# Performance work log

Measured on AMD Instinct MI355X. Metric: run time of the kernel, lower is better.

The kernel has to match this reference:

```python
import jax, jax.numpy as jnp
import numpy as np

B, S, F, OWN, H, E = 16384, 37, 17, 9, 256, 128
NOUT = 7 + 16


def setup_inputs() -> dict:
    key = jax.random.key(0)
    ks = jax.random.split(key, 22)
    obs = jax.random.normal(ks[0], (B, S + 1, F), dtype=jnp.float32)
    pad = jax.random.bernoulli(ks[1], 0.3, (B, S))
    obs = obs.at[:, 1:, :].multiply(jnp.where(pad, 0.0, 1.0)[:, :, None])

    def init(k, shape):
        return jax.random.normal(k, shape, dtype=jnp.float32) * 0.05

    params = dict(
        sW1=init(ks[2], (F, H)), sb1=jnp.zeros((H,), jnp.float32),
        sW2=init(ks[3], (H, H)), sb2=jnp.zeros((H,), jnp.float32),
        sW3=init(ks[4], (H, E)), sb3=jnp.zeros((E,), jnp.float32),
        aW1=init(ks[5], (E + OWN, H)), ab1=jnp.zeros((H,), jnp.float32),
        aW2=init(ks[6], (H, H)), ab2=jnp.zeros((H,), jnp.float32),
        aW3=init(ks[7], (H, NOUT)), ab3=jnp.zeros((NOUT,), jnp.float32),
        vW1=init(ks[8], (E + OWN, H)), vb1=jnp.zeros((H,), jnp.float32),
        vW2=init(ks[9], (H, H)), vb2=jnp.zeros((H,), jnp.float32),
        vW3=init(ks[10], (H, 1)), vb3=jnp.zeros((1,), jnp.float32),
    )
    return {"obs": obs, **params}


def reference(obs, sW1, sb1, sW2, sb2, sW3, sb3,
              aW1, ab1, aW2, ab2, aW3, ab3,
              vW1, vb1, vW2, vb2, vW3, vb3):
    s_own = obs[:, 0, :OWN]                      # [B, 9]
    seqs = obs[:, 1:, :]                         # [B, 37, 17]
    # non-padded mask: rows whose abs-sum is nonzero
    mask = (jnp.sum(jnp.abs(seqs), axis=-1) != 0).astype(obs.dtype)  # [B, 37]

    # shared MLP applied to every row; masked positions zeroed before the
    # pooling sum (equivalent to gather->MLP->scatter into zeros->sum)
    h = jax.nn.relu(seqs @ sW1 + sb1)
    h = jax.nn.relu(h @ sW2 + sb2)
    h = jax.nn.relu(h @ sW3 + sb3)               # [B, 37, E]
    h = h * mask[..., None]
    summed = jnp.sum(h, axis=1)                  # [B, E]

    cat = jnp.concatenate([summed, s_own], axis=1)  # [B, E+9]

    a = jax.nn.relu(cat @ aW1 + ab1)
    a = jax.nn.relu(a @ aW2 + ab2)
    action_logits = a @ aW3 + ab3                # [B, 23]

    v = jax.nn.relu(cat @ vW1 + vb1)
    v = jax.nn.relu(v @ vW2 + vb2)
    value = (v @ vW3 + vb3).reshape(-1)          # [B]

    return action_logits, value
```

## Files before the change

kernel.cpp:

```cpp
#include <hip/hip_runtime.h>
#include <hip/hip_bf16.h>

#define B_    16384
#define S_    37
#define F_    17
#define OWN_  9
#define NOUT_ 23
#define OBS_ROW 646

typedef __bf16 bf16x8 __attribute__((ext_vector_type(8)));
typedef float  f32x4  __attribute__((ext_vector_type(4)));

#define MFMA(a,b,c) __builtin_amdgcn_mfma_f32_16x16x32_bf16(a, b, c, 0, 0, 0)

#define W1F_OFF   0
#define W2F_OFF   8192
#define W3F_OFF   73728
#define AW1F_OFF  106496
#define AW2F_OFF  147456
#define AW3F_OFF  212992
#define VW1F_OFF  221184
#define VW2F_OFF  262144
#define VW3F_OFF  327680
#define PREP_TOTAL 331776

__global__ void prep_kernel(const float* __restrict__ sW1, const float* __restrict__ sW2,
                            const float* __restrict__ sW3, const float* __restrict__ aW1,
                            const float* __restrict__ aW2, const float* __restrict__ aW3,
                            const float* __restrict__ vW1, const float* __restrict__ vW2,
                            const float* __restrict__ vW3, __bf16* __restrict__ ws)
{
    int j = blockIdx.x * 256 + threadIdx.x;
    const float* src; __bf16* dst; int Np, Ks, Ns;
    if (j < 8192)                  { dst = ws + W1F_OFF;  src = sW1; Np = 256; Ks = 17;  Ns = 256; }
    else if ((j -= 8192)  < 65536) { dst = ws + W2F_OFF;  src = sW2; Np = 256; Ks = 256; Ns = 256; }
    else if ((j -= 65536) < 32768) { dst = ws + W3F_OFF;  src = sW3; Np = 128; Ks = 256; Ns = 128; }
    else if ((j -= 32768) < 40960) { dst = ws + AW1F_OFF; src = aW1; Np = 256; Ks = 137; Ns = 256; }
    else if ((j -= 40960) < 65536) { dst = ws + AW2F_OFF; src = aW2; Np = 256; Ks = 256; Ns = 256; }
    else if ((j -= 65536) < 8192)  { dst = ws + AW3F_OFF; src = aW3; Np = 32;  Ks = 256; Ns = 23;  }
    else if ((j -= 8192)  < 40960) { dst = ws + VW1F_OFF; src = vW1; Np = 256; Ks = 137; Ns = 256; }
    else if ((j -= 40960) < 65536) { dst = ws + VW2F_OFF; src = vW2; Np = 256; Ks = 256; Ns = 256; }
    else { j -= 65536;               dst = ws + VW3F_OFF; src = vW3; Np = 16;  Ks = 256; Ns = 1;   }
    const int c = j / (Np * 8), rem = j - c * Np * 8, n = rem >> 3, e = rem & 7, k = c * 8 + e;
    const float v = (k < Ks && n < Ns) ? src[k * Ns + n] : 0.f;
    dst[j] = (__bf16)v;
}

__global__ __launch_bounds__(512, 2) void fused_kernel(
    const float* __restrict__ obs,
    const float* __restrict__ sb1, const float* __restrict__ sb2, const float* __restrict__ sb3,
    const float* __restrict__ ab1, const float* __restrict__ ab2, const float* __restrict__ ab3,
    const float* __restrict__ vb1, const float* __restrict__ vb2, const float* __restrict__ vb3,
    const __bf16* __restrict__ ws, float* __restrict__ out)
{
    __shared__ __align__(16) char pool[74240];
    __bf16* act1 = (__bf16*)pool;
    __bf16* act2 = (__bf16*)(pool + 32768);
    __bf16* xs0  = (__bf16*)(pool + 65536);
    __bf16* xs1  = (__bf16*)(pool + 69632);
    float*  sm0  = (float*)(pool + 73728);
    float*  sm1  = (float*)(pool + 73984);
    __bf16* catf = (__bf16*)(pool + 65536);

    const __bf16* W1f  = ws + W1F_OFF;
    const __bf16* W2f  = ws + W2F_OFF;
    const __bf16* W3f  = ws + W3F_OFF;
    const __bf16* AW1f = ws + AW1F_OFF;
    const __bf16* AW2f = ws + AW2F_OFF;
    const __bf16* AW3f = ws + AW3F_OFF;
    const __bf16* VW1f = ws + VW1F_OFF;
    const __bf16* VW2f = ws + VW2F_OFF;
    const __bf16* VW3f = ws + VW3F_OFF;

    const int tid  = threadIdx.x;
    const int wave = tid >> 6;
    const int lane = tid & 63;
    const int q    = lane >> 4;
    const int l16  = lane & 15;
    const int b0   = blockIdx.x * 16;
    const f32x4 z4 = {0.f, 0.f, 0.f, 0.f};

    for (int i = tid; i < 4096; i += 512) xs0[i] = (__bf16)0.f;

    bf16x8 w1f[2], w2f[8][2], w3f[8];
    float b1v[2], b2v[2];
    #pragma unroll
    for (int nt = 0; nt < 2; ++nt) {
        const int n = wave * 32 + nt * 16 + l16;
        w1f[nt] = *(const bf16x8*)(W1f + ((size_t)q * 256 + n) * 8);
        b1v[nt] = sb1[n];
        b2v[nt] = sb2[n];
        #pragma unroll
        for (int k = 0; k < 8; ++k)
            w2f[k][nt] = *(const bf16x8*)(W2f + ((size_t)(k * 4 + q) * 256 + n) * 8);
    }
    #pragma unroll
    for (int k = 0; k < 8; ++k)
        w3f[k] = *(const bf16x8*)(W3f + ((size_t)(k * 4 + q) * 128 + wave * 16 + l16) * 8);
    const float b3v = sb3[wave * 16 + l16];

    __syncthreads();

    if (wave == 7) {
        const float* p = obs + (size_t)(b0 + (lane & 15)) * OBS_ROW + ((lane >> 4) + 1) * F_;
        float sm = 0.f;
        #pragma unroll
        for (int c = 0; c < F_; ++c) {
            const float v = p[c];
            sm += fabsf(v);
            xs0[((c >> 3) * 64 + lane) * 8 + (c & 7)] = (__bf16)v;
        }
        sm0[lane] = sm;
    }

    f32x4 vsum = z4;

    for (int it = 0; it < 10; ++it) {
        __bf16* xc  = (it & 1) ? xs1 : xs0;
        __bf16* xn  = (it & 1) ? xs0 : xs1;
        float*  smc = (it & 1) ? sm1 : sm0;
        float*  smn = (it & 1) ? sm0 : sm1;

        __syncthreads();

        if (it < 9 && wave == 7) {
            const int s = 4 * (it + 1) + (lane >> 4);
            if (s < S_) {
                const float* p = obs + (size_t)(b0 + (lane & 15)) * OBS_ROW + (s + 1) * F_;
                float sm = 0.f;
                #pragma unroll
                for (int c = 0; c < F_; ++c) {
                    const float v = p[c];
                    sm += fabsf(v);
                    xn[((c >> 3) * 64 + lane) * 8 + (c & 7)] = (__bf16)v;
                }
                smn[lane] = sm;
            } else {
                smn[lane] = 0.f;
            }
        }

        {
            #pragma unroll
            for (int m = 0; m < 4; ++m) {
                const bf16x8 af = *(const bf16x8*)(xc + (q * 64 + m * 16 + l16) * 8);
                #pragma unroll
                for (int nt = 0; nt < 2; ++nt) {
                    const f32x4 h = MFMA(af, w1f[nt], z4);
                    const int n = wave * 32 + nt * 16 + l16, c = n >> 3, e = n & 7;
                    #pragma unroll
                    for (int r = 0; r < 4; ++r) {
                        float v = h[r] + b1v[nt]; v = v > 0.f ? v : 0.f;
                        act1[(c * 64 + m * 16 + q * 4 + r) * 8 + e] = (__bf16)v;
                    }
                }
            }
        }
        __syncthreads();

        {
            f32x4 h2[2][4];
            #pragma unroll
            for (int nt = 0; nt < 2; ++nt)
                #pragma unroll
                for (int m = 0; m < 4; ++m) h2[nt][m] = z4;
            #pragma unroll
            for (int k = 0; k < 8; ++k) {
                const int k8 = k * 4 + q;
                #pragma unroll
                for (int m = 0; m < 4; ++m) {
                    const bf16x8 a = *(const bf16x8*)(act1 + (k8 * 64 + m * 16 + l16) * 8);
                    h2[0][m] = MFMA(a, w2f[k][0], h2[0][m]);
                    h2[1][m] = MFMA(a, w2f[k][1], h2[1][m]);
                }
            }
            #pragma unroll
            for (int nt = 0; nt < 2; ++nt) {
                const int n = wave * 32 + nt * 16 + l16, c = n >> 3, e = n & 7;
                #pragma unroll
                for (int m = 0; m < 4; ++m)
                    #pragma unroll
                    for (int r = 0; r < 4; ++r) {
                        float v = h2[nt][m][r] + b2v[nt]; v = v > 0.f ? v : 0.f;
                        act2[(c * 64 + m * 16 + q * 4 + r) * 8 + e] = (__bf16)v;
                    }
            }
        }
        __syncthreads();

        {
            f32x4 h3[4];
            #pragma unroll
            for (int m = 0; m < 4; ++m) h3[m] = z4;
            #pragma unroll
            for (int k = 0; k < 8; ++k) {
                const int k8 = k * 4 + q;
                #pragma unroll
                for (int m = 0; m < 4; ++m) {
                    const bf16x8 a = *(const bf16x8*)(act2 + (k8 * 64 + m * 16 + l16) * 8);
                    h3[m] = MFMA(a, w3f[k], h3[m]);
                }
            }
            #pragma unroll
            for (int m = 0; m < 4; ++m)
                #pragma unroll
                for (int r = 0; r < 4; ++r) {
                    const float mv = smc[m * 16 + q * 4 + r];
                    float v = h3[m][r] + b3v;
                    v = v > 0.f ? v : 0.f;
                    vsum[r] += (mv != 0.f) ? v : 0.f;
                }
    }
    }

    __syncthreads();

    if (tid < 16) {
        const float* p = obs + (size_t)(b0 + tid) * OBS_ROW;
        #pragma unroll
        for (int c = 0; c < 8; ++c) catf[(16 * 16 + tid) * 8 + c] = (__bf16)p[c];
        catf[(17 * 16 + tid) * 8 + 0] = (__bf16)p[8];
        #pragma unroll
        for (int c = 1; c < 8; ++c) catf[(17 * 16 + tid) * 8 + c] = (__bf16)0.f;
    } else if (tid < 32) {
        const int rr = tid - 16;
        #pragma unroll
        for (int c = 0; c < 8; ++c) {
            catf[(18 * 16 + rr) * 8 + c] = (__bf16)0.f;
            catf[(19 * 16 + rr) * 8 + c] = (__bf16)0.f;
        }
    }
    {
        const int col = wave * 16 + l16, c = col >> 3, e = col & 7;
        #pragma unroll
        for (int r = 0; r < 4; ++r)
            catf[(c * 16 + q * 4 + r) * 8 + e] = (__bf16)vsum[r];
    }
    __syncthreads();

    {
        f32x4 ha[2], hv[2];
        #pragma unroll
        for (int nt = 0; nt < 2; ++nt) { ha[nt] = z4; hv[nt] = z4; }
        #pragma unroll
        for (int k = 0; k < 5; ++k) {
            const int k8 = k * 4 + q;
            const bf16x8 ca = *(const bf16x8*)(catf + (k8 * 16 + l16) * 8);
            #pragma unroll
            for (int nt = 0; nt < 2; ++nt) {
                const int n = wave * 32 + nt * 16 + l16;
                const bf16x8 ba = *(const bf16x8*)(AW1f + ((size_t)k8 * 256 + n) * 8);
                const bf16x8 bv = *(const bf16x8*)(VW1f + ((size_t)k8 * 256 + n) * 8);
                ha[nt] = MFMA(ca, ba, ha[nt]);
                hv[nt] = MFMA(ca, bv, hv[nt]);
            }
        }
        #pragma unroll
        for (int nt = 0; nt < 2; ++nt) {
            const int n = wave * 32 + nt * 16 + l16, c = n >> 3, e = n & 7;
            const float ba_ = ab1[n], bv_ = vb1[n];
            #pragma unroll
            for (int r = 0; r < 4; ++r) {
                float va = ha[nt][r] + ba_; va = va > 0.f ? va : 0.f;
                float vv = hv[nt][r] + bv_; vv = vv > 0.f ? vv : 0.f;
                act1[(c * 64 + q * 4 + r) * 8 + e]      = (__bf16)va;
                act1[(c * 64 + 16 + q * 4 + r) * 8 + e] = (__bf16)vv;
            }
        }
    }
    __syncthreads();

    {
        f32x4 ha[2], hv[2];
        #pragma unroll
        for (int nt = 0; nt < 2; ++nt) { ha[nt] = z4; hv[nt] = z4; }
        #pragma unroll
        for (int k = 0; k < 8; ++k) {
            const int k8 = k * 4 + q;
            const bf16x8 a0 = *(const bf16x8*)(act1 + (k8 * 64 + l16) * 8);
            const bf16x8 a1 = *(const bf16x8*)(act1 + (k8 * 64 + 16 + l16) * 8);
            #pragma unroll
            for (int nt = 0; nt < 2; ++nt) {
                const int n = wave * 32 + nt * 16 + l16;
                const bf16x8 ba = *(const bf16x8*)(AW2f + ((size_t)k8 * 256 + n) * 8);
                const bf16x8 bv = *(const bf16x8*)(VW2f + ((size_t)k8 * 256 + n) * 8);
                ha[nt] = MFMA(a0, ba, ha[nt]);
                hv[nt] = MFMA(a1, bv, hv[nt]);
            }
        }
        #pragma unroll
        for (int nt = 0; nt < 2; ++nt) {
            const int n = wave * 32 + nt * 16 + l16, c = n >> 3, e = n & 7;
            const float ba_ = ab2[n], bv_ = vb2[n];
            #pragma unroll
            for (int r = 0; r < 4; ++r) {
                float va = ha[nt][r] + ba_; va = va > 0.f ? va : 0.f;
                float vv = hv[nt][r] + bv_; vv = vv > 0.f ? vv : 0.f;
                act2[(c * 64 + q * 4 + r) * 8 + e]      = (__bf16)va;
                act2[(c * 64 + 16 + q * 4 + r) * 8 + e] = (__bf16)vv;
            }
        }
    }
    __syncthreads();

    if (wave < 2) {
        f32x4 acc = z4;
        #pragma unroll
        for (int k = 0; k < 8; ++k) {
            const int k8 = k * 4 + q;
            const bf16x8 a0 = *(const bf16x8*)(act2 + (k8 * 64 + l16) * 8);
            const bf16x8 bf = *(const bf16x8*)(AW3f + ((size_t)k8 * 32 + wave * 16 + l16) * 8);
            acc = MFMA(a0, bf, acc);
        }
        const int col = wave * 16 + l16;
        if (col < NOUT_) {
            const float bb = ab3[col];
            #pragma unroll
            for (int r = 0; r < 4; ++r)
                out[(size_t)(b0 + q * 4 + r) * NOUT_ + col] = acc[r] + bb;
        }
    } else if (wave == 2) {
        f32x4 acc = z4;
        #pragma unroll
        for (int k = 0; k < 8; ++k) {
            const int k8 = k * 4 + q;
            const bf16x8 a1 = *(const bf16x8*)(act2 + (k8 * 64 + 16 + l16) * 8);
            const bf16x8 bf = *(const bf16x8*)(VW3f + ((size_t)k8 * 16 + l16) * 8);
            acc = MFMA(a1, bf, acc);
        }
        if (l16 == 0) {
            const float bb = vb3[0];
            #pragma unroll
            for (int r = 0; r < 4; ++r)
                out[(size_t)B_ * NOUT_ + b0 + q * 4 + r] = acc[r] + bb;
        }
    }
}

extern "C" void kernel_launch(void* const* d_in, const int* in_sizes, int n_in,
                              void* d_out, int out_size, void* d_ws, size_t ws_size,
                              hipStream_t stream)
{
    const float* obs = (const float*)d_in[0];
    const float* sW1 = (const float*)d_in[1];
    const float* sb1 = (const float*)d_in[2];
    const float* sW2 = (const float*)d_in[3];
    const float* sb2 = (const float*)d_in[4];
    const float* sW3 = (const float*)d_in[5];
    const float* sb3 = (const float*)d_in[6];
    const float* aW1 = (const float*)d_in[7];
    const float* ab1 = (const float*)d_in[8];
    const float* aW2 = (const float*)d_in[9];
    const float* ab2 = (const float*)d_in[10];
    const float* aW3 = (const float*)d_in[11];
    const float* ab3 = (const float*)d_in[12];
    const float* vW1 = (const float*)d_in[13];
    const float* vb1 = (const float*)d_in[14];
    const float* vW2 = (const float*)d_in[15];
    const float* vb2 = (const float*)d_in[16];
    const float* vW3 = (const float*)d_in[17];
    const float* vb3 = (const float*)d_in[18];

    __bf16* ws = (__bf16*)d_ws;
    float* out = (float*)d_out;

    hipLaunchKernelGGL(prep_kernel, dim3(PREP_TOTAL / 256), dim3(256), 0, stream,
                       sW1, sW2, sW3, aW1, aW2, aW3, vW1, vW2, vW3, ws);
    hipLaunchKernelGGL(fused_kernel, dim3(B_ / 16), dim3(512), 0, stream,
                       obs, sb1, sb2, sb3, ab1, ab2, ab3, vb1, vb2, vb3,
                       (const __bf16*)ws, out);
}
```

Baseline: 283.6 us.

## Preload all obs rows into LDS, transpose MFMA operands, split layer-3 over row halves

All ten groups of neighbor rows for the block are now loaded into shared memory up front, replacing the double-buffered producer wave. The MFMA operand order is swapped so each lane holds four consecutive output features, which allows packed 4-wide bf16 LDS stores and vectorised bias loads. Layer 3 is split so waves cover 32 columns by two row halves, with the partial sums combined through shared memory. This cuts scalar LDS stores and removes the idle producer wave, but raises LDS use to about 107 KB, which may reduce blocks per CU below the launch bound of 2, and the obs load is no longer overlapped with compute.

New measurement: 265.8 us. -6.3%, faster.

```diff
diff --git a/kernel.cpp b/kernel.cpp
--- a/kernel.cpp
+++ b/kernel.cpp
@@ -9,6 +9,7 @@
 #define OBS_ROW 646
 
 typedef __bf16 bf16x8 __attribute__((ext_vector_type(8)));
+typedef __bf16 bf16x4 __attribute__((ext_vector_type(4)));
 typedef float  f32x4  __attribute__((ext_vector_type(4)));
 
 #define MFMA(a,b,c) __builtin_amdgcn_mfma_f32_16x16x32_bf16(a, b, c, 0, 0, 0)
@@ -53,14 +54,13 @@
     const float* __restrict__ vb1, const float* __restrict__ vb2, const float* __restrict__ vb3,
     const __bf16* __restrict__ ws, float* __restrict__ out)
 {
-    __shared__ __align__(16) char pool[74240];
-    __bf16* act1 = (__bf16*)pool;
-    __bf16* act2 = (__bf16*)(pool + 32768);
-    __bf16* xs0  = (__bf16*)(pool + 65536);
-    __bf16* xs1  = (__bf16*)(pool + 69632);
-    float*  sm0  = (float*)(pool + 73728);
-    float*  sm1  = (float*)(pool + 73984);
-    __bf16* catf = (__bf16*)(pool + 65536);
+    __shared__ __align__(16) char pool[109056];
+    __bf16* act1    = (__bf16*)pool;
+    __bf16* act2    = (__bf16*)(pool + 32768);
+    __bf16* xs_full = (__bf16*)(pool + 65536);
+    float*  sm_full = (float*)(pool + 106496);
+    __bf16* catf    = (__bf16*)(pool + 65536);
+    float*  partial = (float*)pool;
 
     const __bf16* W1f  = ws + W1F_OFF;
     const __bf16* W2f  = ws + W2F_OFF;
@@ -77,144 +77,139 @@
     const int lane = tid & 63;
     const int q    = lane >> 4;
     const int l16  = lane & 15;
+    const int qh   = q >> 1;
+    const int e4   = (q & 1) * 4;
     const int b0   = blockIdx.x * 16;
+    const int nc   = wave & 3;
+    const int mr   = wave >> 2;
     const f32x4 z4 = {0.f, 0.f, 0.f, 0.f};
 
-    for (int i = tid; i < 4096; i += 512) xs0[i] = (__bf16)0.f;
-
-    bf16x8 w1f[2], w2f[8][2], w3f[8];
-    float b1v[2], b2v[2];
+    #pragma unroll
+    for (int i = 0; i < 5; ++i)
+        ((f32x4*)xs_full)[tid + i * 512] = z4;
+
+    bf16x8 w1f[2], w2f[8][2], w3f[2][8];
+    f32x4 b1q[2], b2q[2], b3q[2];
     #pragma unroll
     for (int nt = 0; nt < 2; ++nt) {
         const int n = wave * 32 + nt * 16 + l16;
         w1f[nt] = *(const bf16x8*)(W1f + ((size_t)q * 256 + n) * 8);
-        b1v[nt] = sb1[n];
-        b2v[nt] = sb2[n];
-        #pragma unroll
-        for (int k = 0; k < 8; ++k)
+        b1q[nt] = *(const f32x4*)(sb1 + wave * 32 + nt * 16 + q * 4);
+        b2q[nt] = *(const f32x4*)(sb2 + wave * 32 + nt * 16 + q * 4);
+        b3q[nt] = *(const f32x4*)(sb3 + nc * 32 + nt * 16 + q * 4);
+        #pragma unroll
+        for (int k = 0; k < 8; ++k) {
             w2f[k][nt] = *(const bf16x8*)(W2f + ((size_t)(k * 4 + q) * 256 + n) * 8);
-    }
-    #pragma unroll
-    for (int k = 0; k < 8; ++k)
-        w3f[k] = *(const bf16x8*)(W3f + ((size_t)(k * 4 + q) * 128 + wave * 16 + l16) * 8);
-    const float b3v = sb3[wave * 16 + l16];
-
-    __syncthreads();
-
-    if (wave == 7) {
-        const float* p = obs + (size_t)(b0 + (lane & 15)) * OBS_ROW + ((lane >> 4) + 1) * F_;
+            w3f[nt][k] = *(const bf16x8*)(W3f + ((size_t)(k * 4 + q) * 128 + nc * 32 + nt * 16 + l16) * 8);
+        }
+    }
+
+    __syncthreads();
+
+    for (int rr = tid; rr < 640; rr += 512) {
+        const int g = rr >> 6, tr = rr & 63, b = tr & 15, sl = tr >> 4;
+        const int s = g * 4 + sl;
         float sm = 0.f;
-        #pragma unroll
-        for (int c = 0; c < F_; ++c) {
-            const float v = p[c];
-            sm += fabsf(v);
-            xs0[((c >> 3) * 64 + lane) * 8 + (c & 7)] = (__bf16)v;
-        }
-        sm0[lane] = sm;
-    }
-
-    f32x4 vsum = z4;
+        if (s < S_) {
+            const float* p = obs + (size_t)(b0 + b) * OBS_ROW + (s + 1) * F_;
+            #pragma unroll
+            for (int c = 0; c < F_; ++c) {
+                const float v = p[c];
+                sm += fabsf(v);
+                xs_full[g * 2048 + ((c >> 3) * 64 + tr) * 8 + (c & 7)] = (__bf16)v;
+            }
+        }
+        sm_full[rr] = sm;
+    }
+
+    __syncthreads();
+
+    f32x4 vsum[2] = {z4, z4};
 
     for (int it = 0; it < 10; ++it) {
-        __bf16* xc  = (it & 1) ? xs1 : xs0;
-        __bf16* xn  = (it & 1) ? xs0 : xs1;
-        float*  smc = (it & 1) ? sm1 : sm0;
-        float*  smn = (it & 1) ? sm0 : sm1;
-
+        const __bf16* xg  = xs_full + it * 2048;
+        const float*  smg = sm_full + it * 64;
+
+        #pragma unroll
+        for (int m = 0; m < 4; ++m) {
+            const bf16x8 xm = *(const bf16x8*)(xg + (q * 64 + m * 16 + l16) * 8);
+            #pragma unroll
+            for (int nt = 0; nt < 2; ++nt) {
+                const f32x4 h = MFMA(w1f[nt], xm, z4);
+                float v0 = h[0] + b1q[nt][0]; v0 = v0 > 0.f ? v0 : 0.f;
+                float v1 = h[1] + b1q[nt][1]; v1 = v1 > 0.f ? v1 : 0.f;
+                float v2 = h[2] + b1q[nt][2]; v2 = v2 > 0.f ? v2 : 0.f;
+                float v3 = h[3] + b1q[nt][3]; v3 = v3 > 0.f ? v3 : 0.f;
+                const bf16x4 pk = {(__bf16)v0, (__bf16)v1, (__bf16)v2, (__bf16)v3};
+                *(bf16x4*)(act1 + ((wave * 4 + nt * 2 + qh) * 64 + m * 16 + l16) * 8 + e4) = pk;
+            }
+        }
         __syncthreads();
 
-        if (it < 9 && wave == 7) {
-            const int s = 4 * (it + 1) + (lane >> 4);
-            if (s < S_) {
-                const float* p = obs + (size_t)(b0 + (lane & 15)) * OBS_ROW + (s + 1) * F_;
-                float sm = 0.f;
-                #pragma unroll
-                for (int c = 0; c < F_; ++c) {
-                    const float v = p[c];
-                    sm += fabsf(v);
-                    xn[((c >> 3) * 64 + lane) * 8 + (c & 7)] = (__bf16)v;
+        {
+            f32x4 h2[2][4];
+            #pragma unroll
+            for (int nt = 0; nt < 2; ++nt)
+                #pragma unroll
+                for (int m = 0; m < 4; ++m) h2[nt][m] = z4;
+            #pragma unroll
+            for (int k = 0; k < 8; ++k) {
+                const int k8 = k * 4 + q;
+                #pragma unroll
+                for (int m = 0; m < 4; ++m) {
+                    const bf16x8 a = *(const bf16x8*)(act1 + (k8 * 64 + m * 16 + l16) * 8);
+                    h2[0][m] = MFMA(w2f[k][0], a, h2[0][m]);
+                    h2[1][m] = MFMA(w2f[k][1], a, h2[1][m]);
                 }
-                smn[lane] = sm;
-            } else {
-                smn[lane] = 0.f;
-            }
-        }
+            }
+            #pragma unroll
+            for (int nt = 0; nt < 2; ++nt)
+                #pragma unroll
+                for (int m = 0; m < 4; ++m) {
+                    float v0 = h2[nt][m][0] + b2q[nt][0]; v0 = v0 > 0.f ? v0 : 0.f;
+                    float v1 = h2[nt][m][1] + b2q[nt][1]; v1 = v1 > 0.f ? v1 : 0.f;
+                    float v2 = h2[nt][m][2] + b2q[nt][2]; v2 = v2 > 0.f ? v2 : 0.f;
+                    float v3 = h2[nt][m][3] + b2q[nt][3]; v3 = v3 > 0.f ? v3 : 0.f;
+                    const bf16x4 pk = {(__bf16)v0, (__bf16)v1, (__bf16)v2, (__bf16)v3};
+                    *(bf16x4*)(act2 + ((wave * 4 + nt * 2 + qh) * 64 + m * 16 + l16) * 8 + e4) = pk;
+                }
+        }
+        __syncthreads();
 
         {
-            #pragma unroll
-            for (int m = 0; m < 4; ++m) {
-                const bf16x8 af = *(const bf16x8*)(xc + (q * 64 + m * 16 + l16) * 8);
-                #pragma unroll
-                for (int nt = 0; nt < 2; ++nt) {
-                    const f32x4 h = MFMA(af, w1f[nt], z4);
-                    const int n = wave * 32 + nt * 16 + l16, c = n >> 3, e = n & 7;
+            f32x4 h3[2][2] = {{z4, z4}, {z4, z4}};
+            #pragma unroll
+            for (int k = 0; k < 8; ++k) {
+                const int k8 = k * 4 + q;
+                #pragma unroll
+                for (int mi = 0; mi < 2; ++mi) {
+                    const bf16x8 a = *(const bf16x8*)(act2 + (k8 * 64 + (mr * 2 + mi) * 16 + l16) * 8);
+                    h3[0][mi] = MFMA(w3f[0][k], a, h3[0][mi]);
+                    h3[1][mi] = MFMA(w3f[1][k], a, h3[1][mi]);
+                }
+            }
+            #pragma unroll
+            for (int mi = 0; mi < 2; ++mi) {
+                const float mk = (smg[(mr * 2 + mi) * 16 + l16] != 0.f) ? 1.f : 0.f;
+                #pragma unroll
+                for (int nt = 0; nt < 2; ++nt)
                     #pragma unroll
                     for (int r = 0; r < 4; ++r) {
-                        float v = h[r] + b1v[nt]; v = v > 0.f ? v : 0.f;
-                        act1[(c * 64 + m * 16 + q * 4 + r) * 8 + e] = (__bf16)v;
+                        float v = h3[nt][mi][r] + b3q[nt][r];
+                        v = v > 0.f ? v : 0.f;
+                        vsum[nt][r] += mk * v;
                     }
-                }
-            }
-        }
-        __syncthreads();
-
-        {
-            f32x4 h2[2][4];
-            #pragma unroll
-            for (int nt = 0; nt < 2; ++nt)
-                #pragma unroll
-                for (int m = 0; m < 4; ++m) h2[nt][m] = z4;
-            #pragma unroll
-            for (int k = 0; k < 8; ++k) {
-                const int k8 = k * 4 + q;
-                #pragma unroll
-                for (int m = 0; m < 4; ++m) {
-                    const bf16x8 a = *(const bf16x8*)(act1 + (k8 * 64 + m * 16 + l16) * 8);
-                    h2[0][m] = MFMA(a, w2f[k][0], h2[0][m]);
-                    h2[1][m] = MFMA(a, w2f[k][1], h2[1][m]);
-                }
-            }
-            #pragma unroll
-            for (int nt = 0; nt < 2; ++nt) {
-                const int n = wave * 32 + nt * 16 + l16, c = n >> 3, e = n & 7;
-                #pragma unroll
-                for (int m = 0; m < 4; ++m)
-                    #pragma unroll
-                    for (int r = 0; r < 4; ++r) {
-                        float v = h2[nt][m][r] + b2v[nt]; v = v > 0.f ? v : 0.f;
-                        act2[(c * 64 + m * 16 + q * 4 + r) * 8 + e] = (__bf16)v;
-                    }
-            }
-        }
-        __syncthreads();
-
-        {
-            f32x4 h3[4];
-            #pragma unroll
-            for (int m = 0; m < 4; ++m) h3[m] = z4;
-            #pragma unroll
-            for (int k = 0; k < 8; ++k) {
-                const int k8 = k * 4 + q;
-                #pragma unroll
-                for (int m = 0; m < 4; ++m) {
-                    const bf16x8 a = *(const bf16x8*)(act2 + (k8 * 64 + m * 16 + l16) * 8);
-                    h3[m] = MFMA(a, w3f[k], h3[m]);
-                }
-            }
-            #pragma unroll
-            for (int m = 0; m < 4; ++m)
-                #pragma unroll
-                for (int r = 0; r < 4; ++r) {
-                    const float mv = smc[m * 16 + q * 4 + r];
-                    float v = h3[m][r] + b3v;
-                    v = v > 0.f ? v : 0.f;
-                    vsum[r] += (mv != 0.f) ? v : 0.f;
-                }
-    }
-    }
-
-    __syncthreads();
-
+            }
+        }
+    }
+
+    if (mr == 0) {
+        #pragma unroll
+        for (int nt = 0; nt < 2; ++nt)
+            #pragma unroll
+            for (int r = 0; r < 4; ++r)
+                partial[(nc * 32 + nt * 16 + q * 4 + r) * 16 + l16] = vsum[nt][r];
+    }
     if (tid < 16) {
         const float* p = obs + (size_t)(b0 + tid) * OBS_ROW;
         #pragma unroll
@@ -230,18 +225,23 @@
             catf[(19 * 16 + rr) * 8 + c] = (__bf16)0.f;
         }
     }
+    __syncthreads();
+
+    if (mr == 1) {
+        #pragma unroll
+        for (int nt = 0; nt < 2; ++nt) {
+            f32x4 t = vsum[nt];
+            #pragma unroll
+            for (int r = 0; r < 4; ++r)
+                t[r] += partial[(nc * 32 + nt * 16 + q * 4 + r) * 16 + l16];
+            const bf16x4 pk = {(__bf16)t[0], (__bf16)t[1], (__bf16)t[2], (__bf16)t[3]};
+            *(bf16x4*)(catf + ((nc * 4 + nt * 2 + qh) * 16 + l16) * 8 + e4) = pk;
+        }
+    }
+    __syncthreads();
+
     {
-        const int col = wave * 16 + l16, c = col >> 3, e = col & 7;
-        #pragma unroll
-        for (int r = 0; r < 4; ++r)
-            catf[(c * 16 + q * 4 + r) * 8 + e] = (__bf16)vsum[r];
-    }
-    __syncthreads();
-
-    {
-        f32x4 ha[2], hv[2];
-        #pragma unroll
-        for (int nt = 0; nt < 2; ++nt) { ha[nt] = z4; hv[nt] = z4; }
+        f32x4 ha[2] = {z4, z4}, hv[2] = {z4, z4};
         #pragma unroll
         for (int k = 0; k < 5; ++k) {
             const int k8 = k * 4 + q;
@@ -251,29 +251,33 @@
                 const int n = wave * 32 + nt * 16 + l16;
                 const bf16x8 ba = *(const bf16x8*)(AW1f + ((size_t)k8 * 256 + n) * 8);
                 const bf16x8 bv = *(const bf16x8*)(VW1f + ((size_t)k8 * 256 + n) * 8);
-                ha[nt] = MFMA(ca, ba, ha[nt]);
-                hv[nt] = MFMA(ca, bv, hv[nt]);
+                ha[nt] = MFMA(ba, ca, ha[nt]);
+                hv[nt] = MFMA(bv, ca, hv[nt]);
             }
         }
         #pragma unroll
         for (int nt = 0; nt < 2; ++nt) {
-            const int n = wave * 32 + nt * 16 + l16, c = n >> 3, e = n & 7;
-            const float ba_ = ab1[n], bv_ = vb1[n];
-            #pragma unroll
-            for (int r = 0; r < 4; ++r) {
-                float va = ha[nt][r] + ba_; va = va > 0.f ? va : 0.f;
-                float vv = hv[nt][r] + bv_; vv = vv > 0.f ? vv : 0.f;
-                act1[(c * 64 + q * 4 + r) * 8 + e]      = (__bf16)va;
-                act1[(c * 64 + 16 + q * 4 + r) * 8 + e] = (__bf16)vv;
-            }
+            const f32x4 ab_ = *(const f32x4*)(ab1 + wave * 32 + nt * 16 + q * 4);
+            const f32x4 vb_ = *(const f32x4*)(vb1 + wave * 32 + nt * 16 + q * 4);
+            float a0 = ha[nt][0] + ab_[0]; a0 = a0 > 0.f ? a0 : 0.f;
+            float a1 = ha[nt][1] + ab_[1]; a1 = a1 > 0.f ? a1 : 0.f;
+            float a2 = ha[nt][2] + ab_[2]; a2 = a2 > 0.f ? a2 : 0.f;
+            float a3 = ha[nt][3] + ab_[3]; a3 = a3 > 0.f ? a3 : 0.f;
+            float u0 = hv[nt][0] + vb_[0]; u0 = u0 > 0.f ? u0 : 0.f;
+            float u1 = hv[nt][1] + vb_[1]; u1 = u1 > 0.f ? u1 : 0.f;
+            float u2 = hv[nt][2] + vb_[2]; u2 = u2 > 0.f ? u2 : 0.f;
+            float u3 = hv[nt][3] + vb_[3]; u3 = u3 > 0.f ? u3 : 0.f;
+            const bf16x4 pa = {(__bf16)a0, (__bf16)a1, (__bf16)a2, (__bf16)a3};
+            const bf16x4 pv = {(__bf16)u0, (__bf16)u1, (__bf16)u2, (__bf16)u3};
+            const int c = wave * 4 + nt * 2 + qh;
+            *(bf16x4*)(act1 + (c * 64 + l16) * 8 + e4)      = pa;
+            *(bf16x4*)(act1 + (c * 64 + 16 + l16) * 8 + e4) = pv;
         }
     }
     __syncthreads();
 
     {
-        f32x4 ha[2], hv[2];
-        #pragma unroll
-        for (int nt = 0; nt < 2; ++nt) { ha[nt] = z4; hv[nt] = z4; }
+        f32x4 ha[2] = {z4, z4}, hv[2] = {z4, z4};
         #pragma unroll
         for (int k = 0; k < 8; ++k) {
             const int k8 = k * 4 + q;
@@ -284,21 +288,27 @@
                 const int n = wave * 32 + nt * 16 + l16;
                 const bf16x8 ba = *(const bf16x8*)(AW2f + ((size_t)k8 * 256 + n) * 8);
                 const bf16x8 bv = *(const bf16x8*)(VW2f + ((size_t)k8 * 256 + n) * 8);
-                ha[nt] = MFMA(a0, ba, ha[nt]);
-                hv[nt] = MFMA(a1, bv, hv[nt]);
+                ha[nt] = MFMA(ba, a0, ha[nt]);
+                hv[nt] = MFMA(bv, a1, hv[nt]);
             }
         }
         #pragma unroll
         for (int nt = 0; nt < 2; ++nt) {
-            const int n = wave * 32 + nt * 16 + l16, c = n >> 3, e = n & 7;
-            const float ba_ = ab2[n], bv_ = vb2[n];
-            #pragma unroll
-            for (int r = 0; r < 4; ++r) {
-                float va = ha[nt][r] + ba_; va = va > 0.f ? va : 0.f;
-                float vv = hv[nt][r] + bv_; vv = vv > 0.f ? vv : 0.f;
-                act2[(c * 64 + q * 4 + r) * 8 + e]      = (__bf16)va;
-                act2[(c * 64 + 16 + q * 4 + r) * 8 + e] = (__bf16)vv;
-            }
+            const f32x4 ab_ = *(const f32x4*)(ab2 + wave * 32 + nt * 16 + q * 4);
+            const f32x4 vb_ = *(const f32x4*)(vb2 + wave * 32 + nt * 16 + q * 4);
+            float a0 = ha[nt][0] + ab_[0]; a0 = a0 > 0.f ? a0 : 0.f;
+            float a1 = ha[nt][1] + ab_[1]; a1 = a1 > 0.f ? a1 : 0.f;
+            float a2 = ha[nt][2] + ab_[2]; a2 = a2 > 0.f ? a2 : 0.f;
+            float a3 = ha[nt][3] + ab_[3]; a3 = a3 > 0.f ? a3 : 0.f;
+            float u0 = hv[nt][0] + vb_[0]; u0 = u0 > 0.f ? u0 : 0.f;
+            float u1 = hv[nt][1] + vb_[1]; u1 = u1 > 0.f ? u1 : 0.f;
+            float u2 = hv[nt][2] + vb_[2]; u2 = u2 > 0.f ? u2 : 0.f;
+            float u3 = hv[nt][3] + vb_[3]; u3 = u3 > 0.f ? u3 : 0.f;
+            const bf16x4 pa = {(__bf16)a0, (__bf16)a1, (__bf16)a2, (__bf16)a3};
+            const bf16x4 pv = {(__bf16)u0, (__bf16)u1, (__bf16)u2, (__bf16)u3};
+            const int c = wave * 4 + nt * 2 + qh;
+            *(bf16x4*)(act2 + (c * 64 + l16) * 8 + e4)      = pa;
+            *(bf16x4*)(act2 + (c * 64 + 16 + l16) * 8 + e4) = pv;
         }
     }
     __syncthreads();
@@ -310,14 +320,14 @@
             const int k8 = k * 4 + q;
             const bf16x8 a0 = *(const bf16x8*)(act2 + (k8 * 64 + l16) * 8);
             const bf16x8 bf = *(const bf16x8*)(AW3f + ((size_t)k8 * 32 + wave * 16 + l16) * 8);
-            acc = MFMA(a0, bf, acc);
-        }
-        const int col = wave * 16 + l16;
-        if (col < NOUT_) {
-            const float bb = ab3[col];
-            #pragma unroll
-            for (int r = 0; r < 4; ++r)
-                out[(size_t)(b0 + q * 4 + r) * NOUT_ + col] = acc[r] + bb;
+            acc = MFMA(bf, a0, acc);
+        }
+        const int nb = wave * 16 + q * 4;
+        #pragma unroll
+        for (int r = 0; r < 4; ++r) {
+            const int n = nb + r;
+            if (n < NOUT_)
+                out[(size_t)(b0 + l16) * NOUT_ + n] = acc[r] + ab3[n];
         }
     } else if (wave == 2) {
         f32x4 acc = z4;
@@ -326,14 +336,10 @@
             const int k8 = k * 4 + q;
             const bf16x8 a1 = *(const bf16x8*)(act2 + (k8 * 64 + 16 + l16) * 8);
             const bf16x8 bf = *(const bf16x8*)(VW3f + ((size_t)k8 * 16 + l16) * 8);
-            acc = MFMA(a1, bf, acc);
-        }
-        if (l16 == 0) {
-            const float bb = vb3[0];
-            #pragma unroll
-            for (int r = 0; r < 4; ++r)
-                out[(size_t)B_ * NOUT_ + b0 + q * 4 + r] = acc[r] + bb;
-        }
+            acc = MFMA(bf, a1, acc);
+        }
+        if (q == 0)
+            out[(size_t)B_ * NOUT_ + b0 + l16] = acc[0] + vb3[0];
     }
 }
 
```
